# Performance work log

Hardware: AMD Instinct MI355X
Metric: run time of the kernel (lower is better)

The kernel has to match this reference:

```python
import jax, jax.numpy as jnp
import numpy as np

EPS = 1e-4


def setup_inputs() -> dict:
    key = jax.random.key(0)
    k1, k2, k3 = jax.random.split(key, 3)
    B, C, H, W = 8, 3, 1024, 1024
    n_axis, n_knots = 8, 16
    raw = jax.random.uniform(k1, (B, C, H, W), dtype=jnp.float32)
    ys = jax.random.uniform(k2, (B, n_axis, n_knots), dtype=jnp.float32)
    A = jax.random.normal(k3, (B, C, n_axis), dtype=jnp.float32)
    return {"raw": raw, "ys": ys, "A": A}


def reference(raw, ys, A):
    # raw: [B,3,H,W], ys: [B,n_axis,K], A: [B,3,n_axis]
    B, C, H, W = raw.shape
    K = ys.shape[-1]
    pinv_A = jnp.linalg.pinv(A)                      # [B, n_axis, 3]
    mins = jnp.sum(A * (A < 0), axis=1)              # [B, n_axis]
    maxs = jnp.sum(A * (A > 0), axis=1)              # [B, n_axis]

    # project pixels onto axes: [B, n_axis, H, W]
    f = jnp.einsum('bchw,bca->bahw', raw, A)

    # knot x-positions (uniform per batch/axis): [B, n_axis, K+2]
    t = jnp.linspace(0.0, 1.0, K + 2, dtype=raw.dtype)[None, None]
    xs = t * (maxs + EPS - mins)[..., None] + mins[..., None]
    ys_full = jnp.concatenate([mins[..., None], ys, maxs[..., None]], axis=-1)  # [B,A,K+2]
    dx = xs[..., 1] - xs[..., 0]                     # [B, n_axis]
    slopes = jnp.diff(ys_full, axis=-1) / dx[..., None]  # [B, n_axis, K+1]

    # segment index per pixel (replaces masked loop): floor((f - xs0)/dx)
    idx = jnp.clip(jnp.floor((f - mins[..., None, None]) / dx[..., None, None]),
                   0, K).astype(jnp.int32)           # [B, n_axis, H, W]

    idx_flat = idx.reshape(B, -1, H * W)             # [B, n_axis, HW]
    ys_hi = jnp.take_along_axis(ys_full, idx_flat + 1, axis=-1).reshape(f.shape)
    xs_hi = jnp.take_along_axis(xs, idx_flat + 1, axis=-1).reshape(f.shape)
    sl = jnp.take_along_axis(slopes, idx_flat, axis=-1).reshape(f.shape)

    est = ys_hi - (xs_hi - f) * sl                   # [B, n_axis, H, W]

    # project back to RGB: [B, 3, H, W]
    out = jnp.einsum('bahw,bac->bchw', est, pinv_A)
    return out
```

## Files before the change

kernel.cpp:

```cpp
#include <hip/hip_runtime.h>

#define EPS 1e-4f
#define NAXIS 8
#define NKNOTS 16
#define NSEG 17
#define WS_STRIDE 384

__global__ void spline_prep(const float* __restrict__ ys,
                            const float* __restrict__ A,
                            float* __restrict__ ws) {
    const int b = blockIdx.x;
    const float* Ab  = A  + (size_t)b * 3 * NAXIS;
    const float* ysb = ys + (size_t)b * NAXIS * NKNOTS;
    float* w = ws + (size_t)b * WS_STRIDE;
    __shared__ double Ginv[9];
    const int tid = threadIdx.x;

    if (tid == 0) {
        double G[9];
        for (int i = 0; i < 3; ++i)
            for (int j = 0; j < 3; ++j) {
                double s = 0.0;
                for (int a = 0; a < NAXIS; ++a)
                    s += (double)Ab[i * NAXIS + a] * (double)Ab[j * NAXIS + a];
                G[i * 3 + j] = s;
            }
        const double g00 = G[0], g01 = G[1], g02 = G[2];
        const double g11 = G[4], g12 = G[5], g22 = G[8];
        const double det = g00 * (g11 * g22 - g12 * g12)
                         - g01 * (g01 * g22 - g12 * g02)
                         + g02 * (g01 * g12 - g11 * g02);
        const double inv = 1.0 / det;
        Ginv[0] = (g11 * g22 - g12 * g12) * inv;
        Ginv[1] = (g02 * g12 - g01 * g22) * inv;
        Ginv[2] = (g01 * g12 - g02 * g11) * inv;
        Ginv[3] = Ginv[1];
        Ginv[4] = (g00 * g22 - g02 * g02) * inv;
        Ginv[5] = (g02 * g01 - g00 * g12) * inv;
        Ginv[6] = Ginv[2];
        Ginv[7] = Ginv[5];
        Ginv[8] = (g00 * g11 - g01 * g01) * inv;
    }
    __syncthreads();

    if (tid < 24) {
        const int a = tid / 3, c = tid % 3;
        double s = 0.0;
        for (int i = 0; i < 3; ++i)
            s += (double)Ab[i * NAXIS + a] * Ginv[i * 3 + c];
        w[a * 3 + c] = (float)s;
        float mn = 0.f, mx = 0.f;
        for (int i = 0; i < 3; ++i) {
            const float v = Ab[i * NAXIS + a];
            mn += fminf(v, 0.f);
            mx += fmaxf(v, 0.f);
        }
        const float invdx = 17.0f / (mx + EPS - mn);
        w[24 + a * 3 + c] = Ab[c * NAXIS + a] * invdx;
    }
    if (tid < NAXIS) {
        const int a = tid;
        float mn = 0.f, mx = 0.f;
        for (int c = 0; c < 3; ++c) {
            const float v = Ab[c * NAXIS + a];
            mn += fminf(v, 0.f);
            mx += fmaxf(v, 0.f);
        }
        const float range = mx + EPS - mn;
        const float invdx = 17.0f / range;
        w[48 + a] = -mn * invdx;
        float yf[NKNOTS + 2];
        yf[0] = mn;
        for (int k = 0; k < NKNOTS; ++k) yf[k + 1] = ysb[a * NKNOTS + k];
        yf[NKNOTS + 1] = mx;
        for (int s = 0; s < NSEG; ++s) {
            const float dy = yf[s + 1] - yf[s];
            w[64 + (a * NSEG + s) * 2 + 0] = dy;
            w[64 + (a * NSEG + s) * 2 + 1] = yf[s + 1] - (float)(s + 1) * dy;
        }
    }
}

__device__ __forceinline__ float rfl(float x) {
    return __int_as_float(__builtin_amdgcn_readfirstlane(__float_as_int(x)));
}

__global__ __launch_bounds__(256) void spline_main(const float* __restrict__ raw,
                                                   const float* __restrict__ ws,
                                                   float* __restrict__ out,
                                                   int blocksPerBatch, int HW) {
    const int b    = blockIdx.x / blocksPerBatch;
    const int tile = blockIdx.x % blocksPerBatch;

    const float* w = ws + (size_t)b * WS_STRIDE;

    const size_t base = (size_t)b * 3 * HW + (size_t)tile * 1024 + threadIdx.x * 4;
    const float4 r4 = *(const float4*)(raw + base);
    const float4 g4 = *(const float4*)(raw + base + HW);
    const float4 b4 = *(const float4*)(raw + base + 2 * (size_t)HW);

    float cc[56];
    #pragma unroll
    for (int i = 0; i < 14; ++i) {
        const float4 t = *(const float4*)(w + 4 * i);
        cc[4 * i + 0] = rfl(t.x);
        cc[4 * i + 1] = rfl(t.y);
        cc[4 * i + 2] = rfl(t.z);
        cc[4 * i + 3] = rfl(t.w);
    }
    const float* cP = cc;
    const float* cA = cc + 24;
    const float* cO = cc + 48;

    __shared__ float2 sseg[NAXIS * NSEG];
    {
        const float2* wseg = (const float2*)(w + 64);
        for (int i = threadIdx.x; i < NAXIS * NSEG; i += 256)
            sseg[i] = wseg[i];
    }
    __syncthreads();

    float4 o0, o1, o2;
    float* o0p = &o0.x; float* o1p = &o1.x; float* o2p = &o2.x;
    const float* rp = &r4.x; const float* gp = &g4.x; const float* bp = &b4.x;

    #pragma unroll
    for (int p = 0; p < 4; ++p) {
        const float rc = rp[p], gc = gp[p], bc = bp[p];
        float a0 = 0.f, a1 = 0.f, a2 = 0.f;
        #pragma unroll
        for (int a = 0; a < NAXIS; ++a) {
            const float u = fmaf(rc, cA[a * 3 + 0],
                             fmaf(gc, cA[a * 3 + 1],
                             fmaf(bc, cA[a * 3 + 2], cO[a])));
            const int idx = (int)fminf(fmaxf(u, 0.f), 16.0f);
            const float2 ci = sseg[a * NSEG + idx];
            const float est = fmaf(ci.x, u, ci.y);
            a0 = fmaf(est, cP[a * 3 + 0], a0);
            a1 = fmaf(est, cP[a * 3 + 1], a1);
            a2 = fmaf(est, cP[a * 3 + 2], a2);
        }
        o0p[p] = a0; o1p[p] = a1; o2p[p] = a2;
    }

    *(float4*)(out + base)                  = o0;
    *(float4*)(out + base + HW)             = o1;
    *(float4*)(out + base + 2 * (size_t)HW) = o2;
}

extern "C" void kernel_launch(void* const* d_in, const int* in_sizes, int n_in,
                              void* d_out, int out_size, void* d_ws, size_t ws_size,
                              hipStream_t stream) {
    const float* raw = (const float*)d_in[0];
    const float* ys  = (const float*)d_in[1];
    const float* A   = (const float*)d_in[2];
    float* out = (float*)d_out;
    float* ws  = (float*)d_ws;

    const int B  = in_sizes[2] / (3 * NAXIS);
    const int HW = in_sizes[0] / (B * 3);
    const int blocksPerBatch = HW / 1024;

    spline_prep<<<B, 64, 0, stream>>>(ys, A, ws);
    spline_main<<<B * blocksPerBatch, 256, 0, stream>>>(raw, ws, out, blocksPerBatch, HW);
}
```

Measured before the change: 182.1 us.

## Process four tiles per block with software-prefetched loads and nontemporal stores

Each block now handles four 1024-pixel tiles instead of one. It loads the next tile's RGB while computing the current one, and writes outputs with nontemporal stores. This spreads the per-block setup (coefficient loads, shared-memory segment table, barrier) over more pixels and overlaps memory latency with compute. The cost is fewer blocks in the grid and more registers held for the prefetched data.

```diff
diff --git a/kernel.cpp b/kernel.cpp
--- a/kernel.cpp
+++ b/kernel.cpp
@@ -5,6 +5,10 @@
 #define NKNOTS 16
 #define NSEG 17
 #define WS_STRIDE 384
+#define TILES 4
+#define PXB (TILES * 1024)
+
+typedef float fv4 __attribute__((ext_vector_type(4)));
 
 __global__ void spline_prep(const float* __restrict__ ys,
                             const float* __restrict__ A,
@@ -89,20 +93,21 @@
                                                    const float* __restrict__ ws,
                                                    float* __restrict__ out,
                                                    int blocksPerBatch, int HW) {
-    const int b    = blockIdx.x / blocksPerBatch;
-    const int tile = blockIdx.x % blocksPerBatch;
+    const int b   = blockIdx.x / blocksPerBatch;
+    const int blk = blockIdx.x % blocksPerBatch;
 
     const float* w = ws + (size_t)b * WS_STRIDE;
 
-    const size_t base = (size_t)b * 3 * HW + (size_t)tile * 1024 + threadIdx.x * 4;
-    const float4 r4 = *(const float4*)(raw + base);
-    const float4 g4 = *(const float4*)(raw + base + HW);
-    const float4 b4 = *(const float4*)(raw + base + 2 * (size_t)HW);
+    const size_t base0 = (size_t)b * 3 * HW + (size_t)blk * PXB + threadIdx.x * 4;
+
+    fv4 r4 = *(const fv4*)(raw + base0);
+    fv4 g4 = *(const fv4*)(raw + base0 + HW);
+    fv4 b4 = *(const fv4*)(raw + base0 + 2 * (size_t)HW);
 
     float cc[56];
     #pragma unroll
     for (int i = 0; i < 14; ++i) {
-        const float4 t = *(const float4*)(w + 4 * i);
+        const fv4 t = *(const fv4*)(w + 4 * i);
         cc[4 * i + 0] = rfl(t.x);
         cc[4 * i + 1] = rfl(t.y);
         cc[4 * i + 2] = rfl(t.z);
@@ -120,32 +125,44 @@
     }
     __syncthreads();
 
-    float4 o0, o1, o2;
-    float* o0p = &o0.x; float* o1p = &o1.x; float* o2p = &o2.x;
-    const float* rp = &r4.x; const float* gp = &g4.x; const float* bp = &b4.x;
+    #pragma unroll
+    for (int t = 0; t < TILES; ++t) {
+        fv4 rn, gn, bn;
+        if (t + 1 < TILES) {
+            const size_t nb = base0 + (size_t)(t + 1) * 1024;
+            rn = *(const fv4*)(raw + nb);
+            gn = *(const fv4*)(raw + nb + HW);
+            bn = *(const fv4*)(raw + nb + 2 * (size_t)HW);
+        }
 
-    #pragma unroll
-    for (int p = 0; p < 4; ++p) {
-        const float rc = rp[p], gc = gp[p], bc = bp[p];
-        float a0 = 0.f, a1 = 0.f, a2 = 0.f;
+        fv4 o0, o1, o2;
+
         #pragma unroll
-        for (int a = 0; a < NAXIS; ++a) {
-            const float u = fmaf(rc, cA[a * 3 + 0],
-                             fmaf(gc, cA[a * 3 + 1],
-                             fmaf(bc, cA[a * 3 + 2], cO[a])));
-            const int idx = (int)fminf(fmaxf(u, 0.f), 16.0f);
-            const float2 ci = sseg[a * NSEG + idx];
-            const float est = fmaf(ci.x, u, ci.y);
-            a0 = fmaf(est, cP[a * 3 + 0], a0);
-            a1 = fmaf(est, cP[a * 3 + 1], a1);
-            a2 = fmaf(est, cP[a * 3 + 2], a2);
+        for (int p = 0; p < 4; ++p) {
+            const float rc = r4[p], gc = g4[p], bc = b4[p];
+            float a0 = 0.f, a1 = 0.f, a2 = 0.f;
+            #pragma unroll
+            for (int a = 0; a < NAXIS; ++a) {
+                const float u = fmaf(rc, cA[a * 3 + 0],
+                                 fmaf(gc, cA[a * 3 + 1],
+                                 fmaf(bc, cA[a * 3 + 2], cO[a])));
+                const int idx = (int)fminf(fmaxf(u, 0.f), 16.0f);
+                const float2 ci = sseg[a * NSEG + idx];
+                const float est = fmaf(ci.x, u, ci.y);
+                a0 = fmaf(est, cP[a * 3 + 0], a0);
+                a1 = fmaf(est, cP[a * 3 + 1], a1);
+                a2 = fmaf(est, cP[a * 3 + 2], a2);
+            }
+            o0[p] = a0; o1[p] = a1; o2[p] = a2;
         }
-        o0p[p] = a0; o1p[p] = a1; o2p[p] = a2;
+
+        const size_t ob = base0 + (size_t)t * 1024;
+        __builtin_nontemporal_store(o0, (fv4*)(out + ob));
+        __builtin_nontemporal_store(o1, (fv4*)(out + ob + HW));
+        __builtin_nontemporal_store(o2, (fv4*)(out + ob + 2 * (size_t)HW));
+
+        r4 = rn; g4 = gn; b4 = bn;
     }
-
-    *(float4*)(out + base)                  = o0;
-    *(float4*)(out + base + HW)             = o1;
-    *(float4*)(out + base + 2 * (size_t)HW) = o2;
 }
 
 extern "C" void kernel_launch(void* const* d_in, const int* in_sizes, int n_in,
@@ -159,7 +176,7 @@
 
     const int B  = in_sizes[2] / (3 * NAXIS);
     const int HW = in_sizes[0] / (B * 3);
-    const int blocksPerBatch = HW / 1024;
+    const int blocksPerBatch = HW / PXB;
 
     spline_prep<<<B, 64, 0, stream>>>(ys, A, ws);
     spline_main<<<B * blocksPerBatch, 256, 0, stream>>>(raw, ws, out, blocksPerBatch, HW);
```

After: 184.6 us. Within noise of the previous version (+1.4%).
